# Optimization experiments

Hardware: AMD Instinct MI355X
Metric: run time of the kernel (lower is better)

## Reference

```python
import jax, jax.numpy as jnp
import numpy as np


def setup_inputs() -> dict:
    key = jax.random.key(0)
    # x: [B, C, T, M] = [64, 4, 8192, 16]
    x = jax.random.normal(key, (64, 4, 8192, 16), dtype=jnp.float32)
    return {"x": x}


def reference(x) -> jnp.ndarray:
    # torch.cov(row[c].T): variables = last dim M, observations = T, correction=1.
    # Output: [B, C, M, M]
    T = x.shape[2]
    xc = x - jnp.mean(x, axis=2, keepdims=True)        # center over time axis
    cov = jnp.einsum('bctm,bctn->bcmn', xc, xc) / (T - 1)
    return cov
```

## Files before the change

kernel.cpp:

```cpp
#include <hip/hip_runtime.h>


constexpr int T_DIM = 8192;
constexpr int M_DIM = 16;
constexpr int BLOCK = 1024;
constexpr int NWAVE = BLOCK / 64;
constexpr int T_PER_WAVE = T_DIM / NWAVE;
constexpr int ROUNDS = T_PER_WAVE / 32;
constexpr int PF = 4;

using bf16x8 = __attribute__((ext_vector_type(8))) short;
using f32x4  = __attribute__((ext_vector_type(4))) float;

static __device__ inline unsigned pack_bf2(float lo, float hi) {
    union { float f; unsigned u; } a{lo}, b{hi};
    unsigned ra = a.u + 0x7fffu + ((a.u >> 16) & 1u);
    unsigned rb = b.u + 0x7fffu + ((b.u >> 16) & 1u);
    return (ra >> 16) | (rb & 0xffff0000u);
}

__global__ __launch_bounds__(BLOCK)
void cov_kernel(const float* __restrict__ x, float* __restrict__ out) {
    const int bc   = blockIdx.x;
    const int tid  = threadIdx.x;
    const int wave = tid >> 6;
    const int lane = tid & 63;

    const int rg = lane & 15;
    const int g  = lane >> 4;
    const int q  = lane >> 4;
    const int m  = lane & 15;

    __shared__ __align__(16) unsigned stage[NWAVE][2][256];
    __shared__ float Pred[NWAVE][256];
    __shared__ float Sred[NWAVE][M_DIM];
    __shared__ float Stot[M_DIM];

    const float4* __restrict__ xin =
        (const float4*)(x + (size_t)bc * (T_DIM * M_DIM));

    const int idx0 = (wave * T_PER_WAVE + 2 * rg) * 4 + g;

    const int qw = rg >> 2, dq = rg & 3;
    const int roff = (q * 16 + (m ^ q)) * 4;

    f32x4 acc = {0.f, 0.f, 0.f, 0.f};
    float s0 = 0.f, s1 = 0.f, s2 = 0.f, s3 = 0.f;

    float4 buf0[PF], buf1[PF];
#pragma unroll
    for (int r = 0; r < PF; ++r) {
        buf0[r] = xin[idx0 + r * 128];
        buf1[r] = xin[idx0 + r * 128 + 4];
    }

#pragma unroll
    for (int r = 0; r < ROUNDS; ++r) {
        const float4 a0 = buf0[r % PF];
        const float4 a1 = buf1[r % PF];
        if (r + PF < ROUNDS) {
            buf0[r % PF] = xin[idx0 + (r + PF) * 128];
            buf1[r % PF] = xin[idx0 + (r + PF) * 128 + 4];
        }

        s0 += a0.x + a1.x;  s1 += a0.y + a1.y;
        s2 += a0.z + a1.z;  s3 += a0.w + a1.w;
        unsigned* wb = &stage[wave][r & 1][0];
        wb[(qw * 16 + ((4 * g + 0) ^ qw)) * 4 + dq] = pack_bf2(a0.x, a1.x);
        wb[(qw * 16 + ((4 * g + 1) ^ qw)) * 4 + dq] = pack_bf2(a0.y, a1.y);
        wb[(qw * 16 + ((4 * g + 2) ^ qw)) * 4 + dq] = pack_bf2(a0.z, a1.z);
        wb[(qw * 16 + ((4 * g + 3) ^ qw)) * 4 + dq] = pack_bf2(a0.w, a1.w);
        bf16x8 frag = *(const bf16x8*)&stage[wave][r & 1][roff];
        acc = __builtin_amdgcn_mfma_f32_16x16x32_bf16(frag, frag, acc, 0, 0, 0);
    }

#pragma unroll
    for (int off = 1; off <= 8; off <<= 1) {
        s0 += __shfl_xor(s0, off, 64);
        s1 += __shfl_xor(s1, off, 64);
        s2 += __shfl_xor(s2, off, 64);
        s3 += __shfl_xor(s3, off, 64);
    }
    if (rg == 0) {
        Sred[wave][4 * g + 0] = s0;
        Sred[wave][4 * g + 1] = s1;
        Sred[wave][4 * g + 2] = s2;
        Sred[wave][4 * g + 3] = s3;
    }

#pragma unroll
    for (int r = 0; r < 4; ++r)
        Pred[wave][(q * 4 + r) * M_DIM + m] = acc[r];
    __syncthreads();

    if (tid < M_DIM) {
        float s = 0.f;
#pragma unroll
        for (int w = 0; w < NWAVE; ++w) s += Sred[w][tid];
        Stot[tid] = s;
    }
    __syncthreads();

    if (tid < 256) {
        float P = 0.f;
#pragma unroll
        for (int w = 0; w < NWAVE; ++w) P += Pred[w][tid];
        const int mi = tid >> 4;
        const int ni = tid & 15;
        const float cov = (P - Stot[mi] * Stot[ni] * (1.0f / (float)T_DIM))
                        * (1.0f / (float)(T_DIM - 1));
        out[(size_t)bc * 256 + tid] = cov;
    }
}

extern "C" void kernel_launch(void* const* d_in, const int* in_sizes, int n_in,
                              void* d_out, int out_size, void* d_ws, size_t ws_size,
                              hipStream_t stream) {
    const float* x = (const float*)d_in[0];
    float* out = (float*)d_out;
    const int n_bc = in_sizes[0] / (T_DIM * M_DIM);
    cov_kernel<<<dim3(n_bc), dim3(BLOCK), 0, stream>>>(x, out);
}
```

Measured before the change: 185.9 us.

## Split time axis across eight blocks with a second reduction kernel

Each (batch, channel) covariance is now computed by eight 256-thread blocks, each covering a slice of the time axis. Each block writes partial cross-products and column sums to workspace, and a second kernel combines them and applies the mean correction. This is meant to raise the number of blocks and waves in flight so the memory-bound read of the input can use more of the HBM bandwidth. In exchange it adds a second kernel launch and a small global-memory round trip for the partials.

```diff
diff --git a/kernel.cpp b/kernel.cpp
--- a/kernel.cpp
+++ b/kernel.cpp
@@ -1,13 +1,16 @@
 #include <hip/hip_runtime.h>
 
 
-constexpr int T_DIM = 8192;
-constexpr int M_DIM = 16;
-constexpr int BLOCK = 1024;
-constexpr int NWAVE = BLOCK / 64;
-constexpr int T_PER_WAVE = T_DIM / NWAVE;
-constexpr int ROUNDS = T_PER_WAVE / 32;
-constexpr int PF = 4;
+constexpr int T_DIM  = 8192;
+constexpr int M_DIM  = 16;
+constexpr int SLICES = 8;
+constexpr int BLOCK  = 256;
+constexpr int NWAVE  = BLOCK / 64;
+constexpr int ROWS_PER_BLOCK = T_DIM / SLICES;
+constexpr int ROWS_PER_WAVE  = ROWS_PER_BLOCK / NWAVE;
+constexpr int ROUNDS = ROWS_PER_WAVE / 32;
+constexpr int PF     = 4;
+constexpr int WS_STRIDE = 272;
 
 using bf16x8 = __attribute__((ext_vector_type(8))) short;
 using f32x4  = __attribute__((ext_vector_type(4))) float;
@@ -19,12 +22,14 @@
     return (ra >> 16) | (rb & 0xffff0000u);
 }
 
-__global__ __launch_bounds__(BLOCK)
-void cov_kernel(const float* __restrict__ x, float* __restrict__ out) {
-    const int bc   = blockIdx.x;
-    const int tid  = threadIdx.x;
-    const int wave = tid >> 6;
-    const int lane = tid & 63;
+__global__ __launch_bounds__(BLOCK, 6)
+void cov_partial(const float* __restrict__ x, float* __restrict__ ws) {
+    const int blk   = blockIdx.x;
+    const int bc    = blk >> 3;
+    const int slice = blk & 7;
+    const int tid   = threadIdx.x;
+    const int wave  = tid >> 6;
+    const int lane  = tid & 63;
 
     const int rg = lane & 15;
     const int g  = lane >> 4;
@@ -34,12 +39,12 @@
     __shared__ __align__(16) unsigned stage[NWAVE][2][256];
     __shared__ float Pred[NWAVE][256];
     __shared__ float Sred[NWAVE][M_DIM];
-    __shared__ float Stot[M_DIM];
 
     const float4* __restrict__ xin =
         (const float4*)(x + (size_t)bc * (T_DIM * M_DIM));
 
-    const int idx0 = (wave * T_PER_WAVE + 2 * rg) * 4 + g;
+    const int idx0 =
+        (slice * ROWS_PER_BLOCK + wave * ROWS_PER_WAVE + 2 * rg) * 4 + g;
 
     const int qw = rg >> 2, dq = rg & 3;
     const int roff = (q * 16 + (m ^ q)) * 4;
@@ -93,24 +98,42 @@
         Pred[wave][(q * 4 + r) * M_DIM + m] = acc[r];
     __syncthreads();
 
+    float* __restrict__ wsb = ws + (size_t)blk * WS_STRIDE;
+    {
+        const float P = Pred[0][tid] + Pred[1][tid]
+                      + Pred[2][tid] + Pred[3][tid];
+        wsb[tid] = P;
+    }
+    if (tid < M_DIM) {
+        const float S = Sred[0][tid] + Sred[1][tid]
+                      + Sred[2][tid] + Sred[3][tid];
+        wsb[256 + tid] = S;
+    }
+}
+
+__global__ __launch_bounds__(256)
+void cov_final(const float* __restrict__ ws, float* __restrict__ out) {
+    const int bc  = blockIdx.x;
+    const int tid = threadIdx.x;
+    __shared__ float Stot[M_DIM];
+    const float* __restrict__ base = ws + (size_t)bc * SLICES * WS_STRIDE;
     if (tid < M_DIM) {
         float s = 0.f;
 #pragma unroll
-        for (int w = 0; w < NWAVE; ++w) s += Sred[w][tid];
+        for (int sl = 0; sl < SLICES; ++sl)
+            s += base[sl * WS_STRIDE + 256 + tid];
         Stot[tid] = s;
     }
     __syncthreads();
-
-    if (tid < 256) {
-        float P = 0.f;
+    float P = 0.f;
 #pragma unroll
-        for (int w = 0; w < NWAVE; ++w) P += Pred[w][tid];
-        const int mi = tid >> 4;
-        const int ni = tid & 15;
-        const float cov = (P - Stot[mi] * Stot[ni] * (1.0f / (float)T_DIM))
-                        * (1.0f / (float)(T_DIM - 1));
-        out[(size_t)bc * 256 + tid] = cov;
-    }
+    for (int sl = 0; sl < SLICES; ++sl)
+        P += base[sl * WS_STRIDE + tid];
+    const int mi = tid >> 4;
+    const int ni = tid & 15;
+    const float cov = (P - Stot[mi] * Stot[ni] * (1.0f / (float)T_DIM))
+                    * (1.0f / (float)(T_DIM - 1));
+    out[(size_t)bc * 256 + tid] = cov;
 }
 
 extern "C" void kernel_launch(void* const* d_in, const int* in_sizes, int n_in,
@@ -118,6 +141,8 @@
                               hipStream_t stream) {
     const float* x = (const float*)d_in[0];
     float* out = (float*)d_out;
+    float* ws  = (float*)d_ws;
     const int n_bc = in_sizes[0] / (T_DIM * M_DIM);
-    cov_kernel<<<dim3(n_bc), dim3(BLOCK), 0, stream>>>(x, out);
+    cov_partial<<<dim3(n_bc * SLICES), dim3(BLOCK), 0, stream>>>(x, ws);
+    cov_final<<<dim3(n_bc), dim3(256), 0, stream>>>(ws, out);
 }
```

After: 187.3 us. No clear change (+0.8%).
